# Optimization experiments

Measured on AMD Instinct MI355X. Metric: run time of the kernel, lower is better.

The kernel has to match this reference:

```python
import jax, jax.numpy as jnp
import numpy as np
import math

HID = 1152
NH = 16
HD = HID // NH            # 72
P = 2
DEPTH = 4
MLP_M = int(2.0 / 3.0 * int(HID * 4.0))  # 3072 (SwiGLU inner)
FREQ = 256
NCLS = 1000
ROPE_THETA = 10000.0


def rms_norm(x, w, eps=1e-6):
    return x * jax.lax.rsqrt(jnp.mean(jnp.square(x), axis=-1, keepdims=True) + eps) * w


def rotate_half(x):
    # interleaved pairs (a, b) -> (-b, a)
    x2 = x.reshape(x.shape[:-1] + (x.shape[-1] // 2, 2))
    a, b = x2[..., 0], x2[..., 1]
    return jnp.stack((-b, a), axis=-1).reshape(x.shape)


def make_rope(S, head_dim, theta=ROPE_THETA):
    # VisionRotaryEmbedder: per-axis rope dim = head_dim//2, 2 spatial axes concat
    d = head_dim // 2
    f = 1.0 / theta ** (jnp.arange(0, d, 2)[: d // 2].astype(jnp.float32) / d)
    fr = jnp.arange(S, dtype=jnp.float32)[:, None] * f[None, :]   # [S, d//2]
    fr = jnp.repeat(fr, 2, axis=-1)                               # [S, d]
    grid = jnp.concatenate(
        [jnp.broadcast_to(fr[:, None, :], (S, S, d)),
         jnp.broadcast_to(fr[None, :, :], (S, S, d))], axis=-1)   # [S, S, head_dim]
    grid = grid.reshape(S * S, head_dim)
    return jnp.cos(grid), jnp.sin(grid)


def timestep_embedding(t, dim=FREQ, max_period=10000.0):
    half = dim // 2
    freqs = jnp.exp(-math.log(max_period) * jnp.arange(half, dtype=jnp.float32) / half)
    args = t[:, None].astype(jnp.float32) * freqs[None, :]
    return jnp.concatenate([jnp.cos(args), jnp.sin(args)], axis=-1)


def setup_inputs() -> dict:
    key = jax.random.key(0)
    ks = jax.random.split(key, 24)
    s = 0.02
    B, C, H, W = 2, 4, 64, 64
    d = {
        'x': jax.random.normal(ks[0], (B, C, H, W), jnp.float32),
        't': jax.random.uniform(ks[1], (B,), jnp.float32),
        'y': jax.random.randint(ks[2], (B,), 0, NCLS),
        'patch_w': jax.random.normal(ks[3], (P * P * C, HID), jnp.float32) * s,
        'patch_b': jnp.zeros((HID,), jnp.float32),
        't_w1': jax.random.normal(ks[4], (FREQ, HID), jnp.float32) * s,
        't_b1': jnp.zeros((HID,), jnp.float32),
        't_w2': jax.random.normal(ks[5], (HID, HID), jnp.float32) * s,
        't_b2': jnp.zeros((HID,), jnp.float32),
        'y_table': jax.random.normal(ks[6], (NCLS + 1, HID), jnp.float32) * s,
        'norm1_w': jnp.ones((DEPTH, HID), jnp.float32),
        'qkv_w': jax.random.normal(ks[7], (DEPTH, HID, 3 * HID), jnp.float32) * s,
        'qkv_b': jnp.zeros((DEPTH, 3 * HID), jnp.float32),
        'out_w': jax.random.normal(ks[8], (DEPTH, HID, HID), jnp.float32) * s,
        'out_b': jnp.zeros((DEPTH, HID), jnp.float32),
        'norm2_w': jnp.ones((DEPTH, HID), jnp.float32),
        'mlp_w12': jax.random.normal(ks[9], (DEPTH, HID, 2 * MLP_M), jnp.float32) * s,
        'mlp_b12': jnp.zeros((DEPTH, 2 * MLP_M), jnp.float32),
        'mlp_w3': jax.random.normal(ks[10], (DEPTH, MLP_M, HID), jnp.float32) * s,
        'mlp_b3': jnp.zeros((DEPTH, HID), jnp.float32),
        'adaln_w': jax.random.normal(ks[11], (DEPTH, HID, 4 * HID), jnp.float32) * s,
        'adaln_b': jnp.zeros((DEPTH, 4 * HID), jnp.float32),
        'fnorm_w': jnp.ones((HID,), jnp.float32),
        'fadaln_w': jax.random.normal(ks[12], (HID, 2 * HID), jnp.float32) * s,
        'fadaln_b': jnp.zeros((2 * HID,), jnp.float32),
        'flin_w': jax.random.normal(ks[13], (HID, P * P * C), jnp.float32) * s,
        'flin_b': jnp.zeros((P * P * C,), jnp.float32),
    }
    return d


def reference(x, t, y, patch_w, patch_b, t_w1, t_b1, t_w2, t_b2, y_table,
              norm1_w, qkv_w, qkv_b, out_w, out_b, norm2_w,
              mlp_w12, mlp_b12, mlp_w3, mlp_b3, adaln_w, adaln_b,
              fnorm_w, fadaln_w, fadaln_b, flin_w, flin_b):
    B, C, H, W = x.shape
    S = H // P
    L = S * S
    # patchify -> [B, L, P*P*C] -> linear embed
    tok = x.reshape(B, C, S, P, S, P).transpose(0, 2, 4, 3, 5, 1).reshape(B, L, P * P * C)
    h = tok @ patch_w + patch_b
    # conditioning: timestep MLP + class embedding
    temb = timestep_embedding(t)
    temb = jax.nn.silu(temb @ t_w1 + t_b1) @ t_w2 + t_b2
    c = temb + y_table[y]
    c_silu = jax.nn.silu(c)
    cos, sin = make_rope(S, HD)  # [L, HD]
    scale = 1.0 / math.sqrt(HD)

    def block(hx, p):
        n1w, qw, qb, ow, ob, n2w, w12, b12, w3, b3, aw, ab = p
        mod = c_silu @ aw + ab  # [B, 4*HID]
        s_msa, g_msa, s_mlp, g_mlp = jnp.split(mod, 4, axis=-1)
        hmod = rms_norm(hx, n1w) * (1.0 + s_msa[:, None, :])
        qkv = (hmod @ qw + qb).reshape(B, L, 3, NH, HD)
        qkv = jnp.swapaxes(qkv, 1, 3)  # [B, NH, 3, L, HD]
        q, k, v = qkv[:, :, 0], qkv[:, :, 1], qkv[:, :, 2]
        q = q * cos + rotate_half(q) * sin
        k = k * cos + rotate_half(k) * sin
        w = jax.nn.softmax(jnp.einsum('bhqd,bhkd->bhqk', q, k) * scale, axis=-1)
        o = jnp.einsum('bhqk,bhkd->bhqd', w, v)
        o = jnp.swapaxes(o, 1, 2).reshape(B, L, HID) @ ow + ob
        hx = hx + g_msa[:, None, :] * o
        hmod2 = rms_norm(hx, n2w) * (1.0 + s_mlp[:, None, :])
        x12 = hmod2 @ w12 + b12
        x1, x2 = jnp.split(x12, 2, axis=-1)
        m = (jax.nn.silu(x1) * x2) @ w3 + b3
        hx = hx + g_mlp[:, None, :] * m
        return hx, None

    h, _ = jax.lax.scan(block, h, (norm1_w, qkv_w, qkv_b, out_w, out_b, norm2_w,
                                   mlp_w12, mlp_b12, mlp_w3, mlp_b3, adaln_w, adaln_b))

    # final layer: shift+scale modulation then zero-init linear (random here)
    fmod = c_silu @ fadaln_w + fadaln_b
    shift, fscale = jnp.split(fmod, 2, axis=-1)
    hf = rms_norm(h, fnorm_w) * (1.0 + fscale[:, None, :]) + shift[:, None, :]
    out = hf @ flin_w + flin_b  # [B, L, P*P*C]
    out = out.reshape(B, S, S, P, P, C).transpose(0, 5, 1, 3, 2, 4).reshape(B, C, H, W)
    return out
```

## Files before the change

kernel.cpp:

```cpp
#include <hip/hip_runtime.h>
#include <hip/hip_bf16.h>

#define HIDN 1152
#define NHEAD 16
#define HDIM 72
#define LTOK 1024
#define MTOK 2048
#define MLPM 3072

typedef short bf16x8 __attribute__((ext_vector_type(8)));
typedef float f32x4 __attribute__((ext_vector_type(4)));

__device__ __forceinline__ void gload16(const void* g, void* l) {
    __builtin_amdgcn_global_load_lds(
        (const __attribute__((address_space(1))) void*)g,
        (__attribute__((address_space(3))) void*)l,
        16, 0, 0);
}

__device__ __forceinline__ void xcd_swizzle(int& bx, int& by) {
    int gx = gridDim.x;
    int wgid = blockIdx.y * gx + blockIdx.x;
    int cpx = (gx * gridDim.y) >> 3;
    int nid = (wgid & 7) * cpx + (wgid >> 3);
    bx = nid % gx;
    by = nid / gx;
}

__global__ __launch_bounds__(256) void k_patch(const float* __restrict__ x,
        const float* __restrict__ pw, const float* __restrict__ pb,
        float* __restrict__ h) {
    int m = blockIdx.x;
    int b = m >> 10, l = m & 1023;
    int si = l >> 5, sj = l & 31;
    __shared__ float toks[16];
    int tid = threadIdx.x;
    if (tid < 16) {
        int pi = tid >> 3, pj = (tid >> 2) & 1, c = tid & 3;
        toks[tid] = x[((size_t)(b*4 + c)*64 + si*2 + pi)*64 + sj*2 + pj];
    }
    __syncthreads();
    for (int o = tid; o < HIDN; o += 256) {
        float acc = pb[o];
        #pragma unroll
        for (int kk = 0; kk < 16; ++kk) acc += toks[kk] * pw[kk*HIDN + o];
        h[(size_t)m*HIDN + o] = acc;
    }
}

__global__ __launch_bounds__(256) void k_temb1_v2(const float* __restrict__ t,
        const float* __restrict__ w1, const float* __restrict__ b1,
        float* __restrict__ temb1) {
    int jt = blockIdx.x, b = blockIdx.y;
    int tid = threadIdx.x;
    __shared__ float emb[256];
    __shared__ float red[128];
    float tv = t[b];
    if (tid < 128) { float f = __expf(-logf(10000.f) * (float)tid / 128.f);        emb[tid] = cosf(tv * f); }
    else           { float f = __expf(-logf(10000.f) * (float)(tid - 128) / 128.f); emb[tid] = sinf(tv * f); }
    __syncthreads();
    int o = jt*128 + (tid & 127), s = tid >> 7;
    float acc = 0.f;
    for (int k = s*128; k < s*128 + 128; ++k) acc += emb[k] * w1[(size_t)k*HIDN + o];
    if (s) red[tid & 127] = acc;
    __syncthreads();
    if (!s) {
        float v = acc + red[tid] + b1[o];
        temb1[b*HIDN + o] = v / (1.f + __expf(-v));
    }
}

__global__ __launch_bounds__(256) void k_csilu_s1(const float* __restrict__ temb1,
        const float* __restrict__ w2, float* __restrict__ csilup) {
    int jt = blockIdx.x, kz = blockIdx.y;
    int tid = threadIdx.x;
    __shared__ float t1s[2][288];
    __shared__ float red[2][128];
    for (int i = tid; i < 576; i += 256)
        t1s[i/288][i%288] = temb1[(i/288)*HIDN + kz*288 + (i%288)];
    __syncthreads();
    int o = jt*128 + (tid & 127), s = tid >> 7;
    float a0 = 0.f, a1 = 0.f;
    for (int i = s*144; i < s*144 + 144; ++i) {
        float wv = w2[(size_t)(kz*288 + i)*HIDN + o];
        a0 += t1s[0][i]*wv; a1 += t1s[1][i]*wv;
    }
    if (s) { red[0][tid & 127] = a0; red[1][tid & 127] = a1; }
    __syncthreads();
    if (!s) {
        csilup[(kz*2 + 0)*HIDN + o] = a0 + red[0][tid];
        csilup[(kz*2 + 1)*HIDN + o] = a1 + red[1][tid];
    }
}

__global__ __launch_bounds__(128) void k_csilu_s2(const float* __restrict__ csilup,
        const float* __restrict__ b2, const float* __restrict__ ytab,
        const int* __restrict__ y, float* __restrict__ csilu) {
    int o = blockIdx.x*128 + threadIdx.x;
    int b = blockIdx.y;
    float acc = b2[o] + ytab[(size_t)y[b]*HIDN + o];
    #pragma unroll
    for (int kz = 0; kz < 4; ++kz) acc += csilup[(kz*2 + b)*HIDN + o];
    csilu[b*HIDN + o] = acc / (1.f + __expf(-acc));
}

__global__ __launch_bounds__(256) void k_cond_s1(const float* __restrict__ csilu,
        const float* __restrict__ adaln_w, const float* __restrict__ fadaln_w,
        float* __restrict__ condp) {
    int ct = blockIdx.x, kz = blockIdx.y;
    int tid = threadIdx.x;
    int c0 = ct*128;
    const float* Wb; int rstride;
    if (c0 < 18432) { int d = c0/4608; Wb = adaln_w + (size_t)d*HIDN*4608 + (c0 % 4608); rstride = 4608; }
    else            { Wb = fadaln_w + (c0 - 18432); rstride = 2304; }
    __shared__ float cs[2][288];
    __shared__ float red[2][128];
    for (int i = tid; i < 576; i += 256)
        cs[i/288][i%288] = csilu[(i/288)*HIDN + kz*288 + (i%288)];
    __syncthreads();
    int o = tid & 127, s = tid >> 7;
    float a0 = 0.f, a1 = 0.f;
    for (int i = s*144; i < s*144 + 144; ++i) {
        float wv = Wb[(size_t)(kz*288 + i)*rstride + o];
        a0 += cs[0][i]*wv; a1 += cs[1][i]*wv;
    }
    if (s) { red[0][o] = a0; red[1][o] = a1; }
    __syncthreads();
    if (!s) {
        condp[((size_t)kz*2 + 0)*20736 + c0 + o] = a0 + red[0][o];
        condp[((size_t)kz*2 + 1)*20736 + c0 + o] = a1 + red[1][o];
    }
}

__global__ __launch_bounds__(256) void k_cond_s2(const float* __restrict__ condp,
        const float* __restrict__ adaln_b, const float* __restrict__ fadaln_b,
        float* __restrict__ modb, float* __restrict__ fmod) {
    int c = blockIdx.x*256 + threadIdx.x;
    int b = blockIdx.y;
    float acc = 0.f;
    #pragma unroll
    for (int kz = 0; kz < 4; ++kz) acc += condp[((size_t)kz*2 + b)*20736 + c];
    if (c < 18432) {
        int d = c/4608, j = c%4608;
        modb[((size_t)d*2 + b)*4608 + j] = acc + adaln_b[(size_t)d*4608 + j];
    } else {
        int j = c - 18432;
        fmod[(size_t)b*2304 + j] = acc + fadaln_b[j];
    }
}

__global__ __launch_bounds__(256) void k_rope(float* __restrict__ cosb, float* __restrict__ sinb) {
    int idx = blockIdx.x*256 + threadIdx.x;
    if (idx >= LTOK*HDIM) return;
    int l = idx / HDIM, dd = idx % HDIM;
    int i = l >> 5, j = l & 31;
    int pos = (dd < 36) ? i : j;
    int mm = ((dd < 36) ? dd : dd - 36) >> 1;
    float f = __expf(-logf(10000.f) * (float)mm / 18.f);
    float fr = (float)pos * f;
    cosb[idx] = cosf(fr);
    sinb[idx] = sinf(fr);
}

__global__ __launch_bounds__(256) void k_rms(const float* __restrict__ hx,
        const float* __restrict__ nw, const float* __restrict__ smod,
        __hip_bfloat16* __restrict__ outp) {
    int m = blockIdx.x; int b = m >> 10;
    int tid = threadIdx.x;
    const float* row = hx + (size_t)m*HIDN;
    float part = 0.f;
    for (int j = tid; j < HIDN; j += 256) { float v = row[j]; part += v*v; }
    for (int off = 32; off; off >>= 1) part += __shfl_xor(part, off);
    __shared__ float wsum[4];
    if ((tid & 63) == 0) wsum[tid >> 6] = part;
    __syncthreads();
    float rs = rsqrtf((wsum[0]+wsum[1]+wsum[2]+wsum[3]) * (1.f/HIDN) + 1e-6f);
    const float* sb = smod + (size_t)b*4608;
    __hip_bfloat16* orow = outp + (size_t)m*HIDN;
    for (int j = tid; j < HIDN; j += 256)
        orow[j] = __float2bfloat16(row[j] * rs * nw[j] * (1.f + sb[j]));
}

__global__ __launch_bounds__(256) void k_castT_all(
        const float* __restrict__ qkv_w, const float* __restrict__ out_w,
        const float* __restrict__ m12_w, const float* __restrict__ m3_w,
        __hip_bfloat16* __restrict__ wtb) {
    __shared__ float tile[128][65];
    int bid = blockIdx.x;
    int layer = bid / 1944, r = bid % 1944;
    const float* W; __hip_bfloat16* Wt; int K, N, nt, t; bool glu = false;
    __hip_bfloat16* bl = wtb + (size_t)layer*15925248;
    if (r < 486)       { t = r;        nt = 54; K = 1152; N = 3456; W = qkv_w + (size_t)layer*K*N; Wt = bl; }
    else if (r < 648)  { t = r - 486;  nt = 18; K = 1152; N = 1152; W = out_w + (size_t)layer*K*N; Wt = bl + 3981312; }
    else if (r < 1512) { t = r - 648;  nt = 96; K = 1152; N = 6144; W = m12_w + (size_t)layer*K*N; Wt = bl + 5308416; glu = true; }
    else               { t = r - 1512; nt = 18; K = 3072; N = 1152; W = m3_w  + (size_t)layer*K*N; Wt = bl + 12386304; }
    int n0 = (t % nt)*64, k0 = (t / nt)*128;
    int tid = threadIdx.x;
    int rr = tid >> 4, c4 = (tid & 15)*4;
    #pragma unroll
    for (int p = 0; p < 8; ++p) {
        int kk = p*16 + rr;
        float4 v = *(const float4*)(W + (size_t)(k0+kk)*N + n0 + c4);
        tile[kk][c4+0] = v.x; tile[kk][c4+1] = v.y; tile[kk][c4+2] = v.z; tile[kk][c4+3] = v.w;
    }
    __syncthreads();
    int seg = tid & 15, nn0 = tid >> 4;
    #pragma unroll
    for (int p = 0; p < 4; ++p) {
        int nn = p*16 + nn0;
        bf16x8 o;
        #pragma unroll
        for (int j = 0; j < 8; ++j) {
            __hip_bfloat16 hv = __float2bfloat16(tile[seg*8 + j][nn]);
            o[j] = *(short*)&hv;
        }
        int ng = n0 + nn;
        int np = glu ? ((ng < 3072) ? 2*ng : 2*(ng - 3072) + 1) : ng;
        *(bf16x8*)(Wt + (size_t)np*K + k0 + seg*8) = o;
    }
}

template<int EPI, typename OutT>
__global__ __launch_bounds__(256) void k_gemm_bf16(
        const __hip_bfloat16* __restrict__ A,
        const __hip_bfloat16* __restrict__ Wt,
        const float* __restrict__ bias,
        OutT* __restrict__ C, int M, int N, int K,
        const float* __restrict__ gate) {
    __shared__ __hip_bfloat16 Asm[128*64];
    __shared__ __hip_bfloat16 Bsm[128*64];
    int bx, by; xcd_swizzle(bx, by);
    int tid = threadIdx.x;
    int lane = tid & 63, w = tid >> 6;
    int wr = w >> 1, wc = w & 1;
    int m0 = by * 128, n0 = bx * 128;
    f32x4 acc[4][4] = {};
    int lr = lane >> 3, ls = lane & 7;
    int swz = ls ^ (lr & 7);
    int x7 = lane & 7;
    const __hip_bfloat16* Ag = A  + (size_t)(m0 + lr)*K + swz*8;
    const __hip_bfloat16* Bg = Wt + (size_t)(n0 + lr)*K + swz*8;
    for (int k0 = 0; k0 < K; k0 += 64) {
        #pragma unroll
        for (int i = 0; i < 4; ++i) {
            int seg = w*4 + i;
            gload16(Ag + (size_t)(seg*8)*K + k0, (char*)Asm + seg*1024);
            gload16(Bg + (size_t)(seg*8)*K + k0, (char*)Bsm + seg*1024);
        }
        __syncthreads();
        #pragma unroll
        for (int kk = 0; kk < 2; ++kk) {
            bf16x8 af[4], bfr[4];
            #pragma unroll
            for (int m = 0; m < 4; ++m) {
                int row = wr*64 + m*16 + (lane&15);
                af[m] = *(const bf16x8*)(Asm + row*64 + (((kk*4 + (lane>>4)) ^ x7) * 8));
            }
            #pragma unroll
            for (int n = 0; n < 4; ++n) {
                int col = wc*64 + n*16 + (lane&15);
                bfr[n] = *(const bf16x8*)(Bsm + col*64 + (((kk*4 + (lane>>4)) ^ x7) * 8));
            }
            #pragma unroll
            for (int m = 0; m < 4; ++m)
                #pragma unroll
                for (int n = 0; n < 4; ++n)
                    acc[m][n] = __builtin_amdgcn_mfma_f32_16x16x32_bf16(af[m], bfr[n], acc[m][n], 0, 0, 0);
        }
        __syncthreads();
    }
    int r0 = (lane >> 4) * 4;
    int ccol = lane & 15;
    #pragma unroll
    for (int m = 0; m < 4; ++m) {
        #pragma unroll
        for (int rr = 0; rr < 4; ++rr) {
            int row = m0 + wr*64 + m*16 + r0 + rr;
            #pragma unroll
            for (int n = 0; n < 4; ++n) {
                int col = n0 + wc*64 + n*16 + ccol;
                if (EPI == 0) {
                    float val = acc[m][n][rr] + bias[col];
                    C[(size_t)row*N + col] = (OutT)__float2bfloat16(val);
                } else {
                    float val = acc[m][n][rr] + bias[(col & 1) ? 3072 + (col >> 1) : (col >> 1)];
                    float other = __shfl_xor(val, 1);
                    if (!(lane & 1)) {
                        float res = val / (1.f + __expf(-val)) * other;
                        ((__hip_bfloat16*)C)[(size_t)row*(N>>1) + (col>>1)] = __float2bfloat16(res);
                    }
                }
            }
        }
    }
}

__global__ __launch_bounds__(256) void k_gemm_qkv(
        const __hip_bfloat16* __restrict__ A,
        const __hip_bfloat16* __restrict__ Wt,
        const float* __restrict__ bias,
        const float* __restrict__ cosb, const float* __restrict__ sinb,
        __hip_bfloat16* __restrict__ q, __hip_bfloat16* __restrict__ k,
        __hip_bfloat16* __restrict__ v) {
    const int N = 3456, K = HIDN;
    __shared__ __hip_bfloat16 Asm[128*64];
    __shared__ __hip_bfloat16 Bsm[128*64];
    int bx, by; xcd_swizzle(bx, by);
    int tid = threadIdx.x;
    int lane = tid & 63, w = tid >> 6;
    int wr = w >> 1, wc = w & 1;
    int m0 = by * 128, n0 = bx * 128;
    f32x4 acc[4][4] = {};
    int lr = lane >> 3, ls = lane & 7;
    int swz = ls ^ (lr & 7);
    int x7 = lane & 7;
    const __hip_bfloat16* Ag = A  + (size_t)(m0 + lr)*K + swz*8;
    const __hip_bfloat16* Bg = Wt + (size_t)(n0 + lr)*K + swz*8;
    for (int k0 = 0; k0 < K; k0 += 64) {
        #pragma unroll
        for (int i = 0; i < 4; ++i) {
            int seg = w*4 + i;
            gload16(Ag + (size_t)(seg*8)*K + k0, (char*)Asm + seg*1024);
            gload16(Bg + (size_t)(seg*8)*K + k0, (char*)Bsm + seg*1024);
        }
        __syncthreads();
        #pragma unroll
        for (int kk = 0; kk < 2; ++kk) {
            bf16x8 af[4], bfr[4];
            #pragma unroll
            for (int m = 0; m < 4; ++m) {
                int row = wr*64 + m*16 + (lane&15);
                af[m] = *(const bf16x8*)(Asm + row*64 + (((kk*4 + (lane>>4)) ^ x7) * 8));
            }
            #pragma unroll
            for (int n = 0; n < 4; ++n) {
                int col = wc*64 + n*16 + (lane&15);
                bfr[n] = *(const bf16x8*)(Bsm + col*64 + (((kk*4 + (lane>>4)) ^ x7) * 8));
            }
            #pragma unroll
            for (int m = 0; m < 4; ++m)
                #pragma unroll
                for (int n = 0; n < 4; ++n)
                    acc[m][n] = __builtin_amdgcn_mfma_f32_16x16x32_bf16(af[m], bfr[n], acc[m][n], 0, 0, 0);
        }
        __syncthreads();
    }
    int r0 = (lane >> 4) * 4;
    int ccol = lane & 15;
    int sec = n0 / 1152;
    int rembase = n0 - sec*1152 + wc*64;
    #pragma unroll
    for (int m = 0; m < 4; ++m) {
        #pragma unroll
        for (int rr = 0; rr < 4; ++rr) {
            int row = m0 + wr*64 + m*16 + r0 + rr;
            int b = row >> 10, l = row & 1023;
            #pragma unroll
            for (int n = 0; n < 4; ++n) {
                int rem = rembase + n*16 + ccol;
                int h = rem / HDIM, d = rem % HDIM;
                float val = acc[m][n][rr] + bias[sec*1152 + rem];
                if (sec == 2) {
                    v[((size_t)(b*NHEAD + h)*HDIM + d)*LTOK + l] = __float2bfloat16(val);
                } else {
                    float c = cosb[l*HDIM + d], s = sinb[l*HDIM + d];
                    float other = __shfl_xor(val, 1);
                    float res = (d & 1) ? (val*c + other*s) : (val*c - other*s);
                    __hip_bfloat16 hv = __float2bfloat16(res);
                    size_t dst = ((size_t)(b*NHEAD + h)*LTOK + l)*HDIM + d;
                    if (sec == 0) q[dst] = hv; else k[dst] = hv;
                }
            }
        }
    }
}

__global__ __launch_bounds__(256) void k_gemm64(
        const __hip_bfloat16* __restrict__ A,
        const __hip_bfloat16* __restrict__ Wt,
        const float* __restrict__ bias,
        float* __restrict__ C, int M, int N, int K,
        const float* __restrict__ gate) {
    __shared__ __hip_bfloat16 Asm[64*64];
    __shared__ __hip_bfloat16 Bsm[128*64];
    int bx, by; xcd_swizzle(bx, by);
    int tid = threadIdx.x;
    int lane = tid & 63, w = tid >> 6;
    int wr = w >> 1, wc = w & 1;
    int m0 = by * 64, n0 = bx * 128;
    f32x4 acc[2][4] = {};
    int lr = lane >> 3, ls = lane & 7;
    int swz = ls ^ (lr & 7);
    int x7 = lane & 7;
    const __hip_bfloat16* Ag = A  + (size_t)(m0 + lr)*K + swz*8;
    const __hip_bfloat16* Bg = Wt + (size_t)(n0 + lr)*K + swz*8;
    for (int k0 = 0; k0 < K; k0 += 64) {
        #pragma unroll
        for (int i = 0; i < 2; ++i) {
            int seg = w*2 + i;
            gload16(Ag + (size_t)(seg*8)*K + k0, (char*)Asm + seg*1024);
        }
        #pragma unroll
        for (int i = 0; i < 4; ++i) {
            int seg = w*4 + i;
            gload16(Bg + (size_t)(seg*8)*K + k0, (char*)Bsm + seg*1024);
        }
        __syncthreads();
        #pragma unroll
        for (int kk = 0; kk < 2; ++kk) {
            bf16x8 af[2], bfr[4];
            #pragma unroll
            for (int m = 0; m < 2; ++m) {
                int row = wr*32 + m*16 + (lane&15);
                af[m] = *(const bf16x8*)(Asm + row*64 + (((kk*4 + (lane>>4)) ^ x7) * 8));
            }
            #pragma unroll
            for (int n = 0; n < 4; ++n) {
                int col = wc*64 + n*16 + (lane&15);
                bfr[n] = *(const bf16x8*)(Bsm + col*64 + (((kk*4 + (lane>>4)) ^ x7) * 8));
            }
            #pragma unroll
            for (int m = 0; m < 2; ++m)
                #pragma unroll
                for (int n = 0; n < 4; ++n)
                    acc[m][n] = __builtin_amdgcn_mfma_f32_16x16x32_bf16(af[m], bfr[n], acc[m][n], 0, 0, 0);
        }
        __syncthreads();
    }
    int r0 = (lane >> 4) * 4;
    int ccol = lane & 15;
    #pragma unroll
    for (int m = 0; m < 2; ++m) {
        #pragma unroll
        for (int rr = 0; rr < 4; ++rr) {
            int row = m0 + wr*32 + m*16 + r0 + rr;
            int bi = row >> 10;
            #pragma unroll
            for (int n = 0; n < 4; ++n) {
                int col = n0 + wc*64 + n*16 + ccol;
                float val = acc[m][n][rr] + bias[col];
                C[(size_t)row*N + col] += gate[(size_t)bi*4608 + col] * val;
            }
        }
    }
}

__global__ __launch_bounds__(512) void k_attn_mfma(
        const __hip_bfloat16* __restrict__ q,
        const __hip_bfloat16* __restrict__ k,
        const __hip_bfloat16* __restrict__ vt,
        __hip_bfloat16* __restrict__ o) {
    int x = blockIdx.x;
    int head_id = (x & 7)*4 + (x >> 6);
    int qt = (x >> 3) & 7;
    int b = head_id >> 4, h = head_id & 15;
    const float scale = 0.117851130f;
    __shared__ __hip_bfloat16 Ksm[2][64*72];
    __shared__ __hip_bfloat16 Vsm[2][72*64];
    __shared__ __hip_bfloat16 Psm[8][16*72];
    int tid = threadIdx.x, lane = tid & 63, w = tid >> 6;
    int l15 = lane & 15, g = lane >> 4;
    const __hip_bfloat16* qg = q  + ((size_t)(b*NHEAD + h)*LTOK + qt*128)*HDIM;
    const __hip_bfloat16* kg = k  + (size_t)(b*NHEAD + h)*LTOK*HDIM;
    const __hip_bfloat16* vg = vt + (size_t)(b*NHEAD + h)*HDIM*LTOK;
    const bf16x8 z = {};

    bf16x8 qf[3];
    {
        const __hip_bfloat16* qrow = qg + (w*16 + l15)*HDIM;
        qf[0] = *(const bf16x8*)(qrow + g*8);
        qf[1] = *(const bf16x8*)(qrow + 32 + g*8);
        qf[2] = (g == 0) ? *(const bf16x8*)(qrow + 64) : z;
    }
    int vsw  = ((lane & 7) ^ (lane >> 3)) * 8;
    int vrow = lane >> 3;

    f32x4 oacc[5] = {};
    float mold[4] = {-1e30f, -1e30f, -1e30f, -1e30f};
    float lsum[4] = {};

    {
        for (int s = w; s < 9; s += 8) {
            gload16(kg + s*512 + lane*8, (char*)&Ksm[0][0] + s*1024);
            gload16(vg + (size_t)(s*8 + vrow)*LTOK + vsw, (char*)&Vsm[0][0] + s*1024);
        }
    }
    __syncthreads();

    for (int kt2 = 0; kt2 < 16; ++kt2) {
        int cur = kt2 & 1;
        if (kt2 < 15) {
            const __hip_bfloat16* ktg = kg + (size_t)(kt2+1)*64*HDIM;
            const __hip_bfloat16* vtg = vg + (kt2+1)*64;
            for (int s = w; s < 9; s += 8) {
                gload16(ktg + s*512 + lane*8, (char*)&Ksm[cur^1][0] + s*1024);
                gload16(vtg + (size_t)(s*8 + vrow)*LTOK + vsw, (char*)&Vsm[cur^1][0] + s*1024);
            }
        }
        const __hip_bfloat16* Kc = Ksm[cur];
        const __hip_bfloat16* Vc = Vsm[cur];
        f32x4 st[4] = {};
        __builtin_amdgcn_s_setprio(1);
        #pragma unroll
        for (int t = 0; t < 4; ++t) {
            const __hip_bfloat16* krow = Kc + (t*16 + l15)*72;
            bf16x8 kf0 = *(const bf16x8*)(krow + g*8);
            bf16x8 kf1 = *(const bf16x8*)(krow + 32 + g*8);
            bf16x8 kf2 = (g == 0) ? *(const bf16x8*)(krow + 64) : z;
            st[t] = __builtin_amdgcn_mfma_f32_16x16x32_bf16(qf[0], kf0, st[t], 0, 0, 0);
            st[t] = __builtin_amdgcn_mfma_f32_16x16x32_bf16(qf[1], kf1, st[t], 0, 0, 0);
            st[t] = __builtin_amdgcn_mfma_f32_16x16x32_bf16(qf[2], kf2, st[t], 0, 0, 0);
        }
        __builtin_amdgcn_s_setprio(0);
        float mtr[4];
        #pragma unroll
        for (int r = 0; r < 4; ++r) {
            float mt = fmaxf(fmaxf(st[0][r], st[1][r]), fmaxf(st[2][r], st[3][r]));
            mt = fmaxf(mt, __shfl_xor(mt, 1));
            mt = fmaxf(mt, __shfl_xor(mt, 2));
            mt = fmaxf(mt, __shfl_xor(mt, 4));
            mt = fmaxf(mt, __shfl_xor(mt, 8));
            mtr[r] = mt;
        }
        bool need = false;
        #pragma unroll
        for (int r = 0; r < 4; ++r) need |= (mtr[r] - mold[r]) * scale > 8.f;
        if (__any(need)) {
            #pragma unroll
            for (int r = 0; r < 4; ++r) {
                float mn = fmaxf(mold[r], mtr[r]);
                float corr = __expf((mold[r] - mn) * scale);
                mold[r] = mn;
                lsum[r] *= corr;
                #pragma unroll
                for (int dt = 0; dt < 5; ++dt) oacc[dt][r] *= corr;
            }
        }
        #pragma unroll
        for (int r = 0; r < 4; ++r) {
            float rs = 0.f;
            #pragma unroll
            for (int t = 0; t < 4; ++t) {
                float p = __expf((st[t][r] - mold[r]) * scale);
                rs += p;
                Psm[w][(g*4 + r)*72 + t*16 + l15] = __float2bfloat16(p);
            }
            rs += __shfl_xor(rs, 1);
            rs += __shfl_xor(rs, 2);
            rs += __shfl_xor(rs, 4);
            rs += __shfl_xor(rs, 8);
            lsum[r] += rs;
        }
        bf16x8 pa0 = *(const bf16x8*)(&Psm[w][l15*72 + g*8]);
        bf16x8 pa1 = *(const bf16x8*)(&Psm[w][l15*72 + 32 + g*8]);
        int cswz = (l15 & 7)*8;
        __builtin_amdgcn_s_setprio(1);
        #pragma unroll
        for (int dt = 0; dt < 5; ++dt) {
            int row = dt*16 + l15;
            bool valid = (dt < 4) | (l15 < 8);
            bf16x8 vf0 = valid ? *(const bf16x8*)(Vc + row*64 + ((g*8) ^ cswz)) : z;
            bf16x8 vf1 = valid ? *(const bf16x8*)(Vc + row*64 + ((32 + g*8) ^ cswz)) : z;
            oacc[dt] = __builtin_amdgcn_mfma_f32_16x16x32_bf16(pa0, vf0, oacc[dt], 0, 0, 0);
            oacc[dt] = __builtin_amdgcn_mfma_f32_16x16x32_bf16(pa1, vf1, oacc[dt], 0, 0, 0);
        }
        __builtin_amdgcn_s_setprio(0);
        __syncthreads();
    }
    #pragma unroll
    for (int r = 0; r < 4; ++r) {
        float inv = 1.f / lsum[r];
        int row = qt*128 + w*16 + g*4 + r;
        __hip_bfloat16* op = o + ((size_t)b*LTOK + row)*HIDN + h*HDIM;
        #pragma unroll
        for (int dt = 0; dt < 5; ++dt) {
            int d = dt*16 + l15;
            if (d < HDIM) op[d] = __float2bfloat16(oacc[dt][r] * inv);
        }
    }
}

__global__ __launch_bounds__(256) void k_final(const float* __restrict__ hx,
        const float* __restrict__ fnw, const float* __restrict__ fmod,
        const float* __restrict__ flw, const float* __restrict__ flb,
        float* __restrict__ out) {
    int m = blockIdx.x; int b = m >> 10, l = m & 1023;
    int tid = threadIdx.x;
    const float* row = hx + (size_t)m*HIDN;
    float part = 0.f;
    for (int j = tid; j < HIDN; j += 256) { float v2 = row[j]; part += v2*v2; }
    for (int off = 32; off; off >>= 1) part += __shfl_xor(part, off);
    __shared__ float wsum[4];
    __shared__ float hfs[HIDN];
    __shared__ float red[4][16];
    if ((tid & 63) == 0) wsum[tid >> 6] = part;
    __syncthreads();
    float rs = rsqrtf((wsum[0]+wsum[1]+wsum[2]+wsum[3]) * (1.f/HIDN) + 1e-6f);
    const float* fm = fmod + (size_t)b*2304;
    for (int j = tid; j < HIDN; j += 256)
        hfs[j] = row[j] * rs * fnw[j] * (1.f + fm[HIDN + j]) + fm[j];
    __syncthreads();
    float pacc[16] = {};
    for (int j = tid; j < HIDN; j += 256) {
        float hv = hfs[j];
        #pragma unroll
        for (int kk = 0; kk < 16; ++kk) pacc[kk] += hv * flw[j*16 + kk];
    }
    #pragma unroll
    for (int kk = 0; kk < 16; ++kk)
        for (int off = 32; off; off >>= 1) pacc[kk] += __shfl_xor(pacc[kk], off);
    if ((tid & 63) == 0) {
        int w = tid >> 6;
        #pragma unroll
        for (int kk = 0; kk < 16; ++kk) red[w][kk] = pacc[kk];
    }
    __syncthreads();
    if (tid < 16) {
        float val = red[0][tid] + red[1][tid] + red[2][tid] + red[3][tid] + flb[tid];
        int pi = tid >> 3, pj = (tid >> 2) & 1, c = tid & 3;
        int si = l >> 5, sj = l & 31;
        out[((size_t)(b*4 + c)*64 + si*2 + pi)*64 + sj*2 + pj] = val;
    }
}

extern "C" void kernel_launch(void* const* d_in, const int* in_sizes, int n_in,
                              void* d_out, int out_size, void* d_ws, size_t ws_size,
                              hipStream_t stream) {
    const float* x        = (const float*)d_in[0];
    const float* t        = (const float*)d_in[1];
    const int*   y        = (const int*)  d_in[2];
    const float* patch_w  = (const float*)d_in[3];
    const float* patch_b  = (const float*)d_in[4];
    const float* t_w1     = (const float*)d_in[5];
    const float* t_b1     = (const float*)d_in[6];
    const float* t_w2     = (const float*)d_in[7];
    const float* t_b2     = (const float*)d_in[8];
    const float* y_table  = (const float*)d_in[9];
    const float* norm1_w  = (const float*)d_in[10];
    const float* qkv_w    = (const float*)d_in[11];
    const float* qkv_b    = (const float*)d_in[12];
    const float* out_w    = (const float*)d_in[13];
    const float* out_b    = (const float*)d_in[14];
    const float* norm2_w  = (const float*)d_in[15];
    const float* mlp_w12  = (const float*)d_in[16];
    const float* mlp_b12  = (const float*)d_in[17];
    const float* mlp_w3   = (const float*)d_in[18];
    const float* mlp_b3   = (const float*)d_in[19];
    const float* adaln_w  = (const float*)d_in[20];
    const float* adaln_b  = (const float*)d_in[21];
    const float* fnorm_w  = (const float*)d_in[22];
    const float* fadaln_w = (const float*)d_in[23];
    const float* fadaln_b = (const float*)d_in[24];
    const float* flin_w   = (const float*)d_in[25];
    const float* flin_b   = (const float*)d_in[26];

    char* base = (char*)d_ws;
    float*          hx    = (float*)(base);
    __hip_bfloat16* qbf   = (__hip_bfloat16*)(base + 34603008);
    __hip_bfloat16* kbf   = (__hip_bfloat16*)(base + 39321600);
    __hip_bfloat16* vbf   = (__hip_bfloat16*)(base + 44040192);
    __hip_bfloat16* hbf   = (__hip_bfloat16*)(base + 48758784);
    __hip_bfloat16* mhbf  = qbf;
    __hip_bfloat16* wtb   = (__hip_bfloat16*)(base + 53477376);
    float* temb1 = (float*)(base + 180879360);
    float* csilu = (float*)(base + 180888576);
    float* modb  = (float*)(base + 180897792);
    float* fmod  = (float*)(base + 181045248);
    float* cosb  = (float*)(base + 181063680);
    float* sinb  = (float*)(base + 181358592);
    float* condp = (float*)(base + 181653504);
    float* csilup= (float*)(base + 182317056);

    k_patch<<<2048, 256, 0, stream>>>(x, patch_w, patch_b, hx);
    k_temb1_v2<<<dim3(9,2), 256, 0, stream>>>(t, t_w1, t_b1, temb1);
    k_csilu_s1<<<dim3(9,4), 256, 0, stream>>>(temb1, t_w2, csilup);
    k_csilu_s2<<<dim3(9,2), 128, 0, stream>>>(csilup, t_b2, y_table, y, csilu);
    k_cond_s1<<<dim3(162,4), 256, 0, stream>>>(csilu, adaln_w, fadaln_w, condp);
    k_cond_s2<<<dim3(81,2), 256, 0, stream>>>(condp, adaln_b, fadaln_b, modb, fmod);
    k_rope<<<288, 256, 0, stream>>>(cosb, sinb);
    k_castT_all<<<7776, 256, 0, stream>>>(qkv_w, out_w, mlp_w12, mlp_w3, wtb);

    for (int d = 0; d < 4; ++d) {
        const float* modd = modb + (size_t)d*2*4608;
        __hip_bfloat16* wl = wtb + (size_t)d*15925248;
        __hip_bfloat16* wt_qkv = wl;
        __hip_bfloat16* wt_out = wl + 3981312;
        __hip_bfloat16* wt_m12 = wl + 5308416;
        __hip_bfloat16* wt_m3  = wl + 12386304;

        k_rms<<<2048, 256, 0, stream>>>(hx, norm1_w + d*HIDN, modd + 0*HIDN, hbf);
        k_gemm_qkv<<<dim3(27,16), 256, 0, stream>>>(hbf, wt_qkv, qkv_b + d*3456,
                cosb, sinb, qbf, kbf, vbf);
        k_attn_mfma<<<256, 512, 0, stream>>>(qbf, kbf, vbf, hbf);
        k_gemm64<<<dim3(9,32), 256, 0, stream>>>(hbf, wt_out,
                out_b + d*HIDN, hx, MTOK, HIDN, HIDN, modd + 1*HIDN);
        k_rms<<<2048, 256, 0, stream>>>(hx, norm2_w + d*HIDN, modd + 2*HIDN, hbf);
        k_gemm_bf16<2, __hip_bfloat16><<<dim3(48,16), 256, 0, stream>>>(hbf, wt_m12,
                mlp_b12 + d*6144, mhbf, MTOK, 6144, HIDN, nullptr);
        k_gemm64<<<dim3(9,32), 256, 0, stream>>>(mhbf, wt_m3,
                mlp_b3 + d*HIDN, hx, MTOK, HIDN, MLPM, modd + 3*HIDN);
    }
    k_final<<<2048, 256, 0, stream>>>(hx, fnorm_w, fmod, flin_w, flin_b, (float*)d_out);
}
```

Baseline: 1.019 ms.

## Double-buffer LDS in bf16 GEMMs and vectorize RMSNorm row loads

All three bf16 GEMM kernels now use two LDS buffers. The next K-tile's global-to-LDS loads are issued before computing on the current tile, and wave priority is raised around the MFMA block, so load latency overlaps compute. This doubles LDS use per block, which can reduce occupancy. The RMSNorm and final-layer kernels switch to float4 loads held in registers, avoiding a second pass over the row and scalar bf16 stores.

```diff
diff --git a/kernel.cpp b/kernel.cpp
--- a/kernel.cpp
+++ b/kernel.cpp
@@ -16,6 +16,11 @@
         (const __attribute__((address_space(1))) void*)g,
         (__attribute__((address_space(3))) void*)l,
         16, 0, 0);
+}
+
+__device__ __forceinline__ short bfbits(float f) {
+    __hip_bfloat16 h = __float2bfloat16(f);
+    return *(short*)&h;
 }
 
 __device__ __forceinline__ void xcd_swizzle(int& bx, int& by) {
@@ -167,18 +172,37 @@
         __hip_bfloat16* __restrict__ outp) {
     int m = blockIdx.x; int b = m >> 10;
     int tid = threadIdx.x;
-    const float* row = hx + (size_t)m*HIDN;
-    float part = 0.f;
-    for (int j = tid; j < HIDN; j += 256) { float v = row[j]; part += v*v; }
+    const float4* row4 = (const float4*)(hx + (size_t)m*HIDN);
+    float4 v0 = row4[tid];
+    bool extra = tid < 32;
+    float4 v1 = extra ? row4[256 + tid] : make_float4(0.f,0.f,0.f,0.f);
+    float part = v0.x*v0.x + v0.y*v0.y + v0.z*v0.z + v0.w*v0.w
+               + v1.x*v1.x + v1.y*v1.y + v1.z*v1.z + v1.w*v1.w;
     for (int off = 32; off; off >>= 1) part += __shfl_xor(part, off);
     __shared__ float wsum[4];
     if ((tid & 63) == 0) wsum[tid >> 6] = part;
     __syncthreads();
     float rs = rsqrtf((wsum[0]+wsum[1]+wsum[2]+wsum[3]) * (1.f/HIDN) + 1e-6f);
-    const float* sb = smod + (size_t)b*4608;
-    __hip_bfloat16* orow = outp + (size_t)m*HIDN;
-    for (int j = tid; j < HIDN; j += 256)
-        orow[j] = __float2bfloat16(row[j] * rs * nw[j] * (1.f + sb[j]));
+    const float4* nw4 = (const float4*)nw;
+    const float4* sb4 = (const float4*)(smod + (size_t)b*4608);
+    {
+        float4 nv = nw4[tid], sv = sb4[tid];
+        short4 o;
+        o.x = bfbits(v0.x * rs * nv.x * (1.f + sv.x));
+        o.y = bfbits(v0.y * rs * nv.y * (1.f + sv.y));
+        o.z = bfbits(v0.z * rs * nv.z * (1.f + sv.z));
+        o.w = bfbits(v0.w * rs * nv.w * (1.f + sv.w));
+        *(short4*)(outp + (size_t)m*HIDN + tid*4) = o;
+    }
+    if (extra) {
+        float4 nv = nw4[256 + tid], sv = sb4[256 + tid];
+        short4 o;
+        o.x = bfbits(v1.x * rs * nv.x * (1.f + sv.x));
+        o.y = bfbits(v1.y * rs * nv.y * (1.f + sv.y));
+        o.z = bfbits(v1.z * rs * nv.z * (1.f + sv.z));
+        o.w = bfbits(v1.w * rs * nv.w * (1.f + sv.w));
+        *(short4*)(outp + (size_t)m*HIDN + 1024 + tid*4) = o;
+    }
 }
 
 __global__ __launch_bounds__(256) void k_castT_all(
@@ -210,10 +234,7 @@
         int nn = p*16 + nn0;
         bf16x8 o;
         #pragma unroll
-        for (int j = 0; j < 8; ++j) {
-            __hip_bfloat16 hv = __float2bfloat16(tile[seg*8 + j][nn]);
-            o[j] = *(short*)&hv;
-        }
+        for (int j = 0; j < 8; ++j) o[j] = bfbits(tile[seg*8 + j][nn]);
         int ng = n0 + nn;
         int np = glu ? ((ng < 3072) ? 2*ng : 2*(ng - 3072) + 1) : ng;
         *(bf16x8*)(Wt + (size_t)np*K + k0 + seg*8) = o;
@@ -227,8 +248,8 @@
         const float* __restrict__ bias,
         OutT* __restrict__ C, int M, int N, int K,
         const float* __restrict__ gate) {
-    __shared__ __hip_bfloat16 Asm[128*64];
-    __shared__ __hip_bfloat16 Bsm[128*64];
+    __shared__ __hip_bfloat16 Asm[2][128*64];
+    __shared__ __hip_bfloat16 Bsm[2][128*64];
     int bx, by; xcd_swizzle(bx, by);
     int tid = threadIdx.x;
     int lane = tid & 63, w = tid >> 6;
@@ -240,26 +261,40 @@
     int x7 = lane & 7;
     const __hip_bfloat16* Ag = A  + (size_t)(m0 + lr)*K + swz*8;
     const __hip_bfloat16* Bg = Wt + (size_t)(n0 + lr)*K + swz*8;
-    for (int k0 = 0; k0 < K; k0 += 64) {
-        #pragma unroll
-        for (int i = 0; i < 4; ++i) {
-            int seg = w*4 + i;
-            gload16(Ag + (size_t)(seg*8)*K + k0, (char*)Asm + seg*1024);
-            gload16(Bg + (size_t)(seg*8)*K + k0, (char*)Bsm + seg*1024);
-        }
-        __syncthreads();
+    int nk = K >> 6;
+    #pragma unroll
+    for (int i = 0; i < 4; ++i) {
+        int seg = w*4 + i;
+        gload16(Ag + (size_t)(seg*8)*K, (char*)&Asm[0][0] + seg*1024);
+        gload16(Bg + (size_t)(seg*8)*K, (char*)&Bsm[0][0] + seg*1024);
+    }
+    __syncthreads();
+    for (int t = 0; t < nk; ++t) {
+        int cur = t & 1;
+        if (t + 1 < nk) {
+            int k1 = (t + 1) << 6;
+            #pragma unroll
+            for (int i = 0; i < 4; ++i) {
+                int seg = w*4 + i;
+                gload16(Ag + (size_t)(seg*8)*K + k1, (char*)&Asm[cur^1][0] + seg*1024);
+                gload16(Bg + (size_t)(seg*8)*K + k1, (char*)&Bsm[cur^1][0] + seg*1024);
+            }
+        }
+        const __hip_bfloat16* Ac = Asm[cur];
+        const __hip_bfloat16* Bc = Bsm[cur];
+        __builtin_amdgcn_s_setprio(1);
         #pragma unroll
         for (int kk = 0; kk < 2; ++kk) {
             bf16x8 af[4], bfr[4];
             #pragma unroll
             for (int m = 0; m < 4; ++m) {
                 int row = wr*64 + m*16 + (lane&15);
-                af[m] = *(const bf16x8*)(Asm + row*64 + (((kk*4 + (lane>>4)) ^ x7) * 8));
+                af[m] = *(const bf16x8*)(Ac + row*64 + (((kk*4 + (lane>>4)) ^ x7) * 8));
             }
             #pragma unroll
             for (int n = 0; n < 4; ++n) {
                 int col = wc*64 + n*16 + (lane&15);
-                bfr[n] = *(const bf16x8*)(Bsm + col*64 + (((kk*4 + (lane>>4)) ^ x7) * 8));
+                bfr[n] = *(const bf16x8*)(Bc + col*64 + (((kk*4 + (lane>>4)) ^ x7) * 8));
             }
             #pragma unroll
             for (int m = 0; m < 4; ++m)
@@ -267,6 +302,7 @@
                 for (int n = 0; n < 4; ++n)
                     acc[m][n] = __builtin_amdgcn_mfma_f32_16x16x32_bf16(af[m], bfr[n], acc[m][n], 0, 0, 0);
         }
+        __builtin_amdgcn_s_setprio(0);
         __syncthreads();
     }
     int r0 = (lane >> 4) * 4;
@@ -303,8 +339,8 @@
         __hip_bfloat16* __restrict__ q, __hip_bfloat16* __restrict__ k,
         __hip_bfloat16* __restrict__ v) {
     const int N = 3456, K = HIDN;
-    __shared__ __hip_bfloat16 Asm[128*64];
-    __shared__ __hip_bfloat16 Bsm[128*64];
+    __shared__ __hip_bfloat16 Asm[2][128*64];
+    __shared__ __hip_bfloat16 Bsm[2][128*64];
     int bx, by; xcd_swizzle(bx, by);
     int tid = threadIdx.x;
     int lane = tid & 63, w = tid >> 6;
@@ -316,26 +352,40 @@
     int x7 = lane & 7;
     const __hip_bfloat16* Ag = A  + (size_t)(m0 + lr)*K + swz*8;
     const __hip_bfloat16* Bg = Wt + (size_t)(n0 + lr)*K + swz*8;
-    for (int k0 = 0; k0 < K; k0 += 64) {
-        #pragma unroll
-        for (int i = 0; i < 4; ++i) {
-            int seg = w*4 + i;
-            gload16(Ag + (size_t)(seg*8)*K + k0, (char*)Asm + seg*1024);
-            gload16(Bg + (size_t)(seg*8)*K + k0, (char*)Bsm + seg*1024);
-        }
-        __syncthreads();
+    const int nk = K >> 6;
+    #pragma unroll
+    for (int i = 0; i < 4; ++i) {
+        int seg = w*4 + i;
+        gload16(Ag + (size_t)(seg*8)*K, (char*)&Asm[0][0] + seg*1024);
+        gload16(Bg + (size_t)(seg*8)*K, (char*)&Bsm[0][0] + seg*1024);
+    }
+    __syncthreads();
+    for (int t = 0; t < nk; ++t) {
+        int cur = t & 1;
+        if (t + 1 < nk) {
+            int k1 = (t + 1) << 6;
+            #pragma unroll
+            for (int i = 0; i < 4; ++i) {
+                int seg = w*4 + i;
+                gload16(Ag + (size_t)(seg*8)*K + k1, (char*)&Asm[cur^1][0] + seg*1024);
+                gload16(Bg + (size_t)(seg*8)*K + k1, (char*)&Bsm[cur^1][0] + seg*1024);
+            }
+        }
+        const __hip_bfloat16* Ac = Asm[cur];
+        const __hip_bfloat16* Bc = Bsm[cur];
+        __builtin_amdgcn_s_setprio(1);
         #pragma unroll
         for (int kk = 0; kk < 2; ++kk) {
             bf16x8 af[4], bfr[4];
             #pragma unroll
             for (int m = 0; m < 4; ++m) {
                 int row = wr*64 + m*16 + (lane&15);
-                af[m] = *(const bf16x8*)(Asm + row*64 + (((kk*4 + (lane>>4)) ^ x7) * 8));
+                af[m] = *(const bf16x8*)(Ac + row*64 + (((kk*4 + (lane>>4)) ^ x7) * 8));
             }
             #pragma unroll
             for (int n = 0; n < 4; ++n) {
                 int col = wc*64 + n*16 + (lane&15);
-                bfr[n] = *(const bf16x8*)(Bsm + col*64 + (((kk*4 + (lane>>4)) ^ x7) * 8));
+                bfr[n] = *(const bf16x8*)(Bc + col*64 + (((kk*4 + (lane>>4)) ^ x7) * 8));
             }
             #pragma unroll
             for (int m = 0; m < 4; ++m)
@@ -343,6 +393,7 @@
                 for (int n = 0; n < 4; ++n)
                     acc[m][n] = __builtin_amdgcn_mfma_f32_16x16x32_bf16(af[m], bfr[n], acc[m][n], 0, 0, 0);
         }
+        __builtin_amdgcn_s_setprio(0);
         __syncthreads();
     }
     int r0 = (lane >> 4) * 4;
@@ -381,8 +432,8 @@
         const float* __restrict__ bias,
         float* __restrict__ C, int M, int N, int K,
         const float* __restrict__ gate) {
-    __shared__ __hip_bfloat16 Asm[64*64];
-    __shared__ __hip_bfloat16 Bsm[128*64];
+    __shared__ __hip_bfloat16 Asm[2][64*64];
+    __shared__ __hip_bfloat16 Bsm[2][128*64];
     int bx, by; xcd_swizzle(bx, by);
     int tid = threadIdx.x;
     int lane = tid & 63, w = tid >> 6;
@@ -394,30 +445,48 @@
     int x7 = lane & 7;
     const __hip_bfloat16* Ag = A  + (size_t)(m0 + lr)*K + swz*8;
     const __hip_bfloat16* Bg = Wt + (size_t)(n0 + lr)*K + swz*8;
-    for (int k0 = 0; k0 < K; k0 += 64) {
-        #pragma unroll
-        for (int i = 0; i < 2; ++i) {
-            int seg = w*2 + i;
-            gload16(Ag + (size_t)(seg*8)*K + k0, (char*)Asm + seg*1024);
-        }
-        #pragma unroll
-        for (int i = 0; i < 4; ++i) {
-            int seg = w*4 + i;
-            gload16(Bg + (size_t)(seg*8)*K + k0, (char*)Bsm + seg*1024);
-        }
-        __syncthreads();
+    int nk = K >> 6;
+    #pragma unroll
+    for (int i = 0; i < 2; ++i) {
+        int seg = w*2 + i;
+        gload16(Ag + (size_t)(seg*8)*K, (char*)&Asm[0][0] + seg*1024);
+    }
+    #pragma unroll
+    for (int i = 0; i < 4; ++i) {
+        int seg = w*4 + i;
+        gload16(Bg + (size_t)(seg*8)*K, (char*)&Bsm[0][0] + seg*1024);
+    }
+    __syncthreads();
+    for (int t = 0; t < nk; ++t) {
+        int cur = t & 1;
+        if (t + 1 < nk) {
+            int k1 = (t + 1) << 6;
+            #pragma unroll
+            for (int i = 0; i < 2; ++i) {
+                int seg = w*2 + i;
+                gload16(Ag + (size_t)(seg*8)*K + k1, (char*)&Asm[cur^1][0] + seg*1024);
+            }
+            #pragma unroll
+            for (int i = 0; i < 4; ++i) {
+                int seg = w*4 + i;
+                gload16(Bg + (size_t)(seg*8)*K + k1, (char*)&Bsm[cur^1][0] + seg*1024);
+            }
+        }
+        const __hip_bfloat16* Ac = Asm[cur];
+        const __hip_bfloat16* Bc = Bsm[cur];
+        __builtin_amdgcn_s_setprio(1);
         #pragma unroll
         for (int kk = 0; kk < 2; ++kk) {
             bf16x8 af[2], bfr[4];
             #pragma unroll
             for (int m = 0; m < 2; ++m) {
                 int row = wr*32 + m*16 + (lane&15);
-                af[m] = *(const bf16x8*)(Asm + row*64 + (((kk*4 + (lane>>4)) ^ x7) * 8));
+                af[m] = *(const bf16x8*)(Ac + row*64 + (((kk*4 + (lane>>4)) ^ x7) * 8));
             }
             #pragma unroll
             for (int n = 0; n < 4; ++n) {
                 int col = wc*64 + n*16 + (lane&15);
-                bfr[n] = *(const bf16x8*)(Bsm + col*64 + (((kk*4 + (lane>>4)) ^ x7) * 8));
+                bfr[n] = *(const bf16x8*)(Bc + col*64 + (((kk*4 + (lane>>4)) ^ x7) * 8));
             }
             #pragma unroll
             for (int m = 0; m < 2; ++m)
@@ -425,6 +494,7 @@
                 for (int n = 0; n < 4; ++n)
                     acc[m][n] = __builtin_amdgcn_mfma_f32_16x16x32_bf16(af[m], bfr[n], acc[m][n], 0, 0, 0);
         }
+        __builtin_amdgcn_s_setprio(0);
         __syncthreads();
     }
     int r0 = (lane >> 4) * 4;
@@ -586,9 +656,12 @@
         float* __restrict__ out) {
     int m = blockIdx.x; int b = m >> 10, l = m & 1023;
     int tid = threadIdx.x;
-    const float* row = hx + (size_t)m*HIDN;
-    float part = 0.f;
-    for (int j = tid; j < HIDN; j += 256) { float v2 = row[j]; part += v2*v2; }
+    const float4* row4 = (const float4*)(hx + (size_t)m*HIDN);
+    float4 v0 = row4[tid];
+    bool extra = tid < 32;
+    float4 v1 = extra ? row4[256 + tid] : make_float4(0.f,0.f,0.f,0.f);
+    float part = v0.x*v0.x + v0.y*v0.y + v0.z*v0.z + v0.w*v0.w
+               + v1.x*v1.x + v1.y*v1.y + v1.z*v1.z + v1.w*v1.w;
     for (int off = 32; off; off >>= 1) part += __shfl_xor(part, off);
     __shared__ float wsum[4];
     __shared__ float hfs[HIDN];
@@ -596,9 +669,27 @@
     if ((tid & 63) == 0) wsum[tid >> 6] = part;
     __syncthreads();
     float rs = rsqrtf((wsum[0]+wsum[1]+wsum[2]+wsum[3]) * (1.f/HIDN) + 1e-6f);
-    const float* fm = fmod + (size_t)b*2304;
-    for (int j = tid; j < HIDN; j += 256)
-        hfs[j] = row[j] * rs * fnw[j] * (1.f + fm[HIDN + j]) + fm[j];
+    const float4* fn4 = (const float4*)fnw;
+    const float4* sh4 = (const float4*)(fmod + (size_t)b*2304);
+    const float4* fs4 = (const float4*)(fmod + (size_t)b*2304 + HIDN);
+    {
+        float4 nv = fn4[tid], sc = fs4[tid], sh = sh4[tid];
+        float4 hv;
+        hv.x = v0.x * rs * nv.x * (1.f + sc.x) + sh.x;
+        hv.y = v0.y * rs * nv.y * (1.f + sc.y) + sh.y;
+        hv.z = v0.z * rs * nv.z * (1.f + sc.z) + sh.z;
+        hv.w = v0.w * rs * nv.w * (1.f + sc.w) + sh.w;
+        *(float4*)&hfs[tid*4] = hv;
+    }
+    if (extra) {
+        float4 nv = fn4[256+tid], sc = fs4[256+tid], sh = sh4[256+tid];
+        float4 hv;
+        hv.x = v1.x * rs * nv.x * (1.f + sc.x) + sh.x;
+        hv.y = v1.y * rs * nv.y * (1.f + sc.y) + sh.y;
+        hv.z = v1.z * rs * nv.z * (1.f + sc.z) + sh.z;
+        hv.w = v1.w * rs * nv.w * (1.f + sc.w) + sh.w;
+        *(float4*)&hfs[1024 + tid*4] = hv;
+    }
     __syncthreads();
     float pacc[16] = {};
     for (int j = tid; j < HIDN; j += 256) {
```

Result: no change. 1.015 ms (-0.4%).
